# Kernel tuning notes

Hardware: AMD Instinct MI355X
Metric: run time of the kernel (lower is better)

The kernel has to match this reference:

```python
import jax, jax.numpy as jnp
import numpy as np

EPS = 1e-5

def setup_inputs() -> dict:
    key = jax.random.key(0)
    ks = jax.random.split(key, 12)
    b, C, Hx = 8, 1024, 28          # x: (b, C, Hx, Hx); y: (b, C//2, 2*Hx, 2*Hx)
    C2 = C // 2
    r = C2 // 7                      # fc bottleneck = 73
    f32 = jnp.float32
    inp = {
        'y': jax.random.normal(ks[0], (b, C2, 2*Hx, 2*Hx), f32),
        'x': jax.random.normal(ks[1], (b, C, Hx, Hx), f32),
        'fc1_w': jax.random.normal(ks[2], (r, C2), f32) * 0.02,
        'fc2_w': jax.random.normal(ks[3], (C2, r), f32) * 0.02,
        'conv_w': jax.random.normal(ks[4], (C2, C, 1, 1), f32) * 0.02,
        'conv_b': jnp.zeros((C2,), f32),
        'conv1_w': jax.random.normal(ks[5], (C2, C2 * 4, 1, 1), f32) * 0.02,
        'conv1_b': jnp.zeros((C2,), f32),
        'bn_gamma': jnp.ones((C2,), f32),
        'bn_beta': jnp.zeros((C2,), f32),
        'bn_mean': jnp.zeros((C2,), f32),
        'bn_var': jnp.ones((C2,), f32),
        'dw_w': jax.random.normal(ks[6], (C, 1, 3, 3), f32) * 0.1,  # depthwise, groups=C
        'dw_b': jnp.zeros((C,), f32),
    }
    return inp

def reference(y, x, fc1_w, fc2_w, conv_w, conv_b, conv1_w, conv1_b,
              bn_gamma, bn_beta, bn_mean, bn_var, dw_w, dw_b):
    def bn(t):  # BatchNorm2d in eval mode (running stats); same bn module reused twice
        return (t - bn_mean[:, None, None]) * jax.lax.rsqrt(bn_var[:, None, None] + EPS) \
               * bn_gamma[:, None, None] + bn_beta[:, None, None]
    # SE channel attention on y
    s = jnp.mean(y, axis=(2, 3))                              # (b, C2) GAP
    s = jax.nn.relu(s @ fc1_w.T) @ fc2_w.T                    # bias-free FCs
    y1 = y * jax.nn.sigmoid(s)[:, :, None, None]
    # depthwise 3x3 conv on x
    x1 = jax.lax.conv_general_dilated(
        x, dw_w, (1, 1), ((1, 1), (1, 1)),
        feature_group_count=x.shape[1],
        dimension_numbers=('NCHW', 'OIHW', 'NCHW')) + dw_b[None, :, None, None]
    # np.cov per (b, c) map: rows are variables, ddof=1 -> (Xc @ Xc^T)/(W-1)
    Wn = x1.shape[-1]
    xc = x1 - jnp.mean(x1, axis=-1, keepdims=True)
    x2 = jnp.einsum('bchw,bcgw->bchg', xc, xc) / (Wn - 1)     # (b, C, H, H)
    # 1x1 conv C->C2, bn, sigmoid
    x2 = jnp.einsum('bchw,oc->bohw', x2, conv_w[:, :, 0, 0]) + conv_b[None, :, None, None]
    x2 = jax.nn.sigmoid(bn(x2))
    # bilinear upsample x2 (half-pixel == torch align_corners=False)
    def up2(t):
        bb, cc, hh, ww = t.shape
        return jax.image.resize(t, (bb, cc, 2 * hh, 2 * ww), method='bilinear')
    x_up = up2(x)
    x2_up = up2(x2)
    cat = jnp.concatenate([y1, x2_up, x_up], axis=1)          # (b, 4*C2, 2H, 2W)
    out = jnp.einsum('bchw,oc->bohw', cat, conv1_w[:, :, 0, 0]) + conv1_b[None, :, None, None]
    return jax.nn.relu(bn(out))
```

## Files before the change

### kernel.cpp

```cpp
#include <hip/hip_runtime.h>
#include <math.h>

#define EPSV 1e-5f
#define B 8
#define C 1024
#define C2 512
#define RK 73
#define HW 784
#define QW 3136

typedef __attribute__((ext_vector_type(8))) short bf16x8;
typedef __attribute__((ext_vector_type(4))) float f32x4;

__device__ __forceinline__ unsigned short f2bf(float f) {
    unsigned u = __float_as_uint(f);
    return (unsigned short)((u + 0x7fffu + ((u >> 16) & 1u)) >> 16);
}
__device__ __forceinline__ float ld_f(const float* p) { return *p; }
__device__ __forceinline__ float ld_f(const unsigned short* p) {
    return __uint_as_float(((unsigned)*p) << 16);
}

__global__ void gap_kernel(const float* __restrict__ y, float* __restrict__ s0) {
    int bc = blockIdx.x;
    const float* p = y + (size_t)bc * QW;
    float sum = 0.f;
    for (int i = threadIdx.x; i < QW; i += 256) sum += p[i];
    for (int off = 32; off > 0; off >>= 1) sum += __shfl_down(sum, off, 64);
    __shared__ float red[4];
    if ((threadIdx.x & 63) == 0) red[threadIdx.x >> 6] = sum;
    __syncthreads();
    if (threadIdx.x == 0)
        s0[bc] = (red[0] + red[1] + red[2] + red[3]) * (1.0f / QW);
}

__global__ void se_fc_kernel(const float* __restrict__ s0,
                             const float* __restrict__ fc1_w,
                             const float* __restrict__ fc2_w,
                             float* __restrict__ att) {
    int b = blockIdx.x;
    __shared__ float sv[C2];
    __shared__ float hv[RK];
    for (int i = threadIdx.x; i < C2; i += 256) sv[i] = s0[b * C2 + i];
    __syncthreads();
    if (threadIdx.x < RK) {
        float acc = 0.f;
        const float* wr = fc1_w + threadIdx.x * C2;
        for (int k = 0; k < C2; ++k) acc += wr[k] * sv[k];
        hv[threadIdx.x] = fmaxf(acc, 0.f);
    }
    __syncthreads();
    for (int o = threadIdx.x; o < C2; o += 256) {
        float acc = 0.f;
        const float* wr = fc2_w + o * RK;
        for (int j = 0; j < RK; ++j) acc += wr[j] * hv[j];
        att[b * C2 + o] = 1.f / (1.f + expf(-acc));
    }
}

__global__ void dwcov_kernel(const float* __restrict__ x,
                             const float* __restrict__ dw_w,
                             const float* __restrict__ dw_b,
                             unsigned short* __restrict__ cov) {
    int bc = blockIdx.x;
    int c = bc & (C - 1);
    __shared__ float xs[HW];
    __shared__ float x1[HW];
    __shared__ float rm[28];
    const float* px = x + (size_t)bc * HW;
    for (int i = threadIdx.x; i < HW; i += 256) xs[i] = px[i];
    float wk[9];
#pragma unroll
    for (int j = 0; j < 9; ++j) wk[j] = dw_w[c * 9 + j];
    float bias = dw_b[c];
    __syncthreads();
    for (int p = threadIdx.x; p < HW; p += 256) {
        int h = p / 28, w = p - h * 28;
        float acc = bias;
#pragma unroll
        for (int dh = 0; dh < 3; ++dh) {
            int hh = h + dh - 1;
            if (hh < 0 || hh >= 28) continue;
#pragma unroll
            for (int dw = 0; dw < 3; ++dw) {
                int ww = w + dw - 1;
                if (ww < 0 || ww >= 28) continue;
                acc += xs[hh * 28 + ww] * wk[dh * 3 + dw];
            }
        }
        x1[p] = acc;
    }
    __syncthreads();
    if (threadIdx.x < 28) {
        float s = 0.f;
        for (int w = 0; w < 28; ++w) s += x1[threadIdx.x * 28 + w];
        rm[threadIdx.x] = s * (1.f / 28.f);
    }
    __syncthreads();
    unsigned short* pc = cov + (size_t)bc * HW;
    for (int p = threadIdx.x; p < HW; p += 256) {
        int h = p / 28, g = p - h * 28;
        float mh = rm[h], mg = rm[g];
        float acc = 0.f;
        for (int w = 0; w < 28; ++w)
            acc += (x1[h * 28 + w] - mh) * (x1[g * 28 + w] - mg);
        pc[p] = f2bf(acc * (1.f / 27.f));
    }
}

__global__ void pack_w(const float* __restrict__ conv_w, const float* __restrict__ conv_b,
                       const float* __restrict__ conv1_w, const float* __restrict__ conv1_b,
                       const float* __restrict__ bn_g, const float* __restrict__ bn_b,
                       const float* __restrict__ bn_m, const float* __restrict__ bn_v,
                       const float* __restrict__ att,
                       unsigned short* __restrict__ w0b, unsigned short* __restrict__ w1y,
                       unsigned short* __restrict__ w1pT,
                       float* __restrict__ sA, float* __restrict__ sB0, float* __restrict__ sB1) {
    int o = blockIdx.x, t = threadIdx.x;
    for (int i = t; i < C; i += 256) w0b[(size_t)o * C + i] = f2bf(conv_w[(size_t)o * C + i]);
    for (int i = t; i < 1536; i += 256) w1pT[(size_t)o * 1536 + i] = f2bf(conv1_w[(size_t)o * 2048 + 512 + i]);
#pragma unroll
    for (int b = 0; b < B; ++b)
        for (int c = t; c < C2; c += 256)
            w1y[((size_t)b * C2 + o) * C2 + c] = f2bf(conv1_w[(size_t)o * 2048 + c] * att[b * C2 + c]);
    if (t == 0) {
        float sc = rsqrtf(bn_v[o] + EPSV) * bn_g[o];
        float bi = bn_b[o] - bn_m[o] * sc;
        sA[o] = sc;
        sB0[o] = conv_b[o] * sc + bi;
        sB1[o] = conv1_b[o] * sc + bi;
    }
}

__global__ __launch_bounds__(256)
void transpose_pass(const float* __restrict__ src, unsigned short* __restrict__ dst,
                    int rows, int cols, int dpitch, int doff) {
    int b = blockIdx.z;
    int c0 = blockIdx.y * 64, p0 = blockIdx.x * 64;
    __shared__ float ts[64][65];
    int tid = threadIdx.x;
    int pl = tid & 63, r0 = tid >> 6;
    const float* sb = src + ((size_t)b * rows + c0) * cols + p0;
    if (p0 + pl < cols) {
#pragma unroll
        for (int j = 0; j < 16; ++j) {
            int cl = r0 + j * 4;
            ts[cl][pl] = sb[(size_t)cl * cols + pl];
        }
    }
    __syncthreads();
    int cl = tid & 63;
#pragma unroll
    for (int j = 0; j < 16; ++j) {
        int pl2 = r0 + j * 4;
        if (p0 + pl2 < cols)
            dst[((size_t)b * cols + p0 + pl2) * dpitch + doff + c0 + cl] = f2bf(ts[cl][pl2]);
    }
}

template<int MODE, int K>
__global__ __launch_bounds__(256)
void mfma_gemm(const unsigned short* __restrict__ wpk,
               const void* __restrict__ bsrc_v,
               const unsigned short* __restrict__ Pb,
               const float* __restrict__ sA, const float* __restrict__ sB,
               void* __restrict__ outv) {
    constexpr int NIT = K / 32;
    constexpr int NT  = (MODE == 2) ? 49 : 98;
    constexpr int TPC = (NT + 7) / 8;
    int bx = blockIdx.x;
    int r = bx & 7, i = bx >> 3;
    int t = r * TPC + (i >> 3);
    if (t >= NT) return;
    int o0 = (i & 7) * 64;
    int n0 = t * 64;
    int b = blockIdx.z;
    union SM {
        struct { __align__(16) unsigned short Wt[2][2560]; __align__(16) unsigned short At[2][2560]; } s;
        float pt[(MODE == 2) ? 64 * 84 : 4];
    };
    __shared__ SM sm;
    int tid = threadIdx.x;
    int lane = tid & 63, wv = tid >> 6;
    int ln = lane & 15, quad = lane >> 4;
    int o_w = (wv >> 1) * 32, q_w = (wv & 1) * 32;
    int swr = tid >> 2, swk = (tid & 3) * 8;
    int s_gq = tid & 63, s_gk8 = tid >> 6;
    int qg = n0 + s_gq;
    const unsigned short* wp = (MODE == 2) ? wpk + (size_t)b * C2 * C2 : wpk;
    const unsigned short* wg = wp + (size_t)(o0 + swr) * K + swk;
    const unsigned short* bg_s = nullptr;
    const unsigned short* bg_c = nullptr;
    const float* bg_f = nullptr;
    if (MODE == 0) {
        int bq = qg / HW, pp = qg - bq * HW;
        bg_s = (const unsigned short*)bsrc_v + ((size_t)bq * C + s_gk8 * 8) * HW + pp;
    } else if (MODE == 1) {
        bg_c = (const unsigned short*)bsrc_v + (size_t)(n0 + swr) * K + swk;
    } else {
        bg_f = (const float*)bsrc_v + ((size_t)b * C2 + s_gk8 * 8) * QW + qg;
    }

    {
        float4 wv4 = *(const float4*)wg;
        *(float4*)&sm.s.Wt[0][swr * 40 + swk] = wv4;
        unsigned short pk[8];
        if (MODE == 0) {
#pragma unroll
            for (int j = 0; j < 8; ++j) pk[j] = bg_s[(size_t)j * HW];
            *(float4*)&sm.s.At[0][s_gq * 40 + s_gk8 * 8] = *(float4*)pk;
        } else if (MODE == 1) {
            *(float4*)&sm.s.At[0][swr * 40 + swk] = *(const float4*)bg_c;
        } else {
#pragma unroll
            for (int j = 0; j < 8; ++j) pk[j] = f2bf(bg_f[(size_t)j * QW]);
            *(float4*)&sm.s.At[0][s_gq * 40 + s_gk8 * 8] = *(float4*)pk;
        }
    }
    __syncthreads();

    f32x4 acc[2][2] = {};
    for (int i2 = 0; i2 < NIT; ++i2) {
        int cur = i2 & 1;
        float4 wn;
        unsigned short bn[8];
        if (i2 + 1 < NIT) {
            wn = *(const float4*)(wg + (size_t)(i2 + 1) * 32);
            if (MODE == 0) {
                const unsigned short* s = bg_s + (size_t)(i2 + 1) * 32 * HW;
#pragma unroll
                for (int j = 0; j < 8; ++j) bn[j] = s[(size_t)j * HW];
            } else if (MODE == 1) {
                *(float4*)bn = *(const float4*)(bg_c + (size_t)(i2 + 1) * 32);
            } else {
                const float* s = bg_f + (size_t)(i2 + 1) * 32 * QW;
#pragma unroll
                for (int j = 0; j < 8; ++j) bn[j] = f2bf(s[(size_t)j * QW]);
            }
        }
        bf16x8 af[2], bfr[2];
#pragma unroll
        for (int mt = 0; mt < 2; ++mt)
            af[mt] = *(const bf16x8*)&sm.s.Wt[cur][(o_w + mt * 16 + ln) * 40 + quad * 8];
#pragma unroll
        for (int nt = 0; nt < 2; ++nt)
            bfr[nt] = *(const bf16x8*)&sm.s.At[cur][(q_w + nt * 16 + ln) * 40 + quad * 8];
#pragma unroll
        for (int mt = 0; mt < 2; ++mt)
#pragma unroll
            for (int nt = 0; nt < 2; ++nt)
                acc[mt][nt] = __builtin_amdgcn_mfma_f32_16x16x32_bf16(af[mt], bfr[nt], acc[mt][nt], 0, 0, 0);
        if (i2 + 1 < NIT) {
            int nxt = cur ^ 1;
            *(float4*)&sm.s.Wt[nxt][swr * 40 + swk] = wn;
            if (MODE == 1) *(float4*)&sm.s.At[nxt][swr * 40 + swk] = *(float4*)bn;
            else           *(float4*)&sm.s.At[nxt][s_gq * 40 + s_gk8 * 8] = *(float4*)bn;
            __syncthreads();
        }
    }

    if (MODE == 2) {
        float* outp = (float*)outv;
        __syncthreads();
        int h0 = n0 / 56;
        int hmin = (h0 & 1) ? (h0 >> 1) : max(0, (h0 >> 1) - 1);
        for (int e = tid; e < 64 * 84; e += 256) {
            int o_l = e / 84, rem = e - o_l * 84;
            int s = rem / 28, w = rem - s * 28;
            int row = min(hmin + s, 27);
            sm.pt[e] = ld_f(&Pb[((size_t)b * C2 + o0 + o_l) * HW + row * 28 + w]);
        }
        __syncthreads();
#pragma unroll
        for (int nt = 0; nt < 2; ++nt) {
            int q = n0 + q_w + nt * 16 + ln;
            int hq = q / 56, wq = q - hq * 56;
            int hm = hq >> 1, wm = wq >> 1;
            int hn = (hq & 1) ? min(hm + 1, 27) : max(hm - 1, 0);
            int wn_ = (wq & 1) ? min(wm + 1, 27) : max(wm - 1, 0);
            int rm_ = (hm - hmin) * 28, rn_ = (hn - hmin) * 28;
#pragma unroll
            for (int mt = 0; mt < 2; ++mt)
#pragma unroll
                for (int reg = 0; reg < 4; ++reg) {
                    int ol = o_w + mt * 16 + quad * 4 + reg;
                    int o = o0 + ol;
                    const float* Pt = &sm.pt[ol * 84];
                    float up = 0.5625f * Pt[rm_ + wm] + 0.1875f * (Pt[rm_ + wn_] + Pt[rn_ + wm])
                             + 0.0625f * Pt[rn_ + wn_];
                    float v = (acc[mt][nt][reg] + up) * sA[o] + sB[o];
                    outp[((size_t)b * C2 + o) * QW + q] = fmaxf(v, 0.f);
                }
        }
    } else if (MODE == 0) {
        unsigned short* outp = (unsigned short*)outv;
#pragma unroll
        for (int nt = 0; nt < 2; ++nt) {
            int n = n0 + q_w + nt * 16 + ln;
#pragma unroll
            for (int mt = 0; mt < 2; ++mt) {
                int ob = o0 + o_w + mt * 16 + quad * 4;
                unsigned short pk[4];
#pragma unroll
                for (int reg = 0; reg < 4; ++reg) {
                    int o = ob + reg;
                    float v = acc[mt][nt][reg] * sA[o] + sB[o];
                    pk[reg] = f2bf(1.f / (1.f + expf(-v)));
                }
                *(uint2*)&outp[(size_t)n * 1536 + ob] = *(uint2*)pk;
            }
        }
    } else {
        unsigned short* outp = (unsigned short*)outv;
#pragma unroll
        for (int nt = 0; nt < 2; ++nt) {
            int n = n0 + q_w + nt * 16 + ln;
            int be = n / HW, pe = n - be * HW;
#pragma unroll
            for (int mt = 0; mt < 2; ++mt)
#pragma unroll
                for (int reg = 0; reg < 4; ++reg) {
                    int o = o0 + o_w + mt * 16 + quad * 4 + reg;
                    outp[((size_t)be * C2 + o) * HW + pe] = f2bf(acc[mt][nt][reg]);
                }
        }
    }
}

extern "C" void kernel_launch(void* const* d_in, const int* in_sizes, int n_in,
                              void* d_out, int out_size, void* d_ws, size_t ws_size,
                              hipStream_t stream) {
    const float* y       = (const float*)d_in[0];
    const float* x       = (const float*)d_in[1];
    const float* fc1_w   = (const float*)d_in[2];
    const float* fc2_w   = (const float*)d_in[3];
    const float* conv_w  = (const float*)d_in[4];
    const float* conv_b  = (const float*)d_in[5];
    const float* conv1_w = (const float*)d_in[6];
    const float* conv1_b = (const float*)d_in[7];
    const float* bn_g    = (const float*)d_in[8];
    const float* bn_b    = (const float*)d_in[9];
    const float* bn_m    = (const float*)d_in[10];
    const float* bn_v    = (const float*)d_in[11];
    const float* dw_w    = (const float*)d_in[12];
    const float* dw_b    = (const float*)d_in[13];
    float* out = (float*)d_out;

    float* ws  = (float*)d_ws;
    float* s0  = ws;
    float* att = ws + 4096;
    float* sA  = ws + 8192;
    float* sB0 = ws + 8704;
    float* sB1 = ws + 9216;
    unsigned short* w0b    = (unsigned short*)(ws + 9728);
    unsigned short* w1y    = w0b + (size_t)C2 * C;
    unsigned short* w1pT   = w1y + (size_t)B * C2 * C2;
    unsigned short* cov_bf = w1pT + (size_t)C2 * 1536;
    unsigned short* BcatT  = cov_bf + (size_t)B * C * HW;
    unsigned short* Pb     = BcatT + (size_t)B * HW * 1536;

    gap_kernel<<<B * C2, 256, 0, stream>>>(y, s0);
    se_fc_kernel<<<B, 256, 0, stream>>>(s0, fc1_w, fc2_w, att);
    pack_w<<<C2, 256, 0, stream>>>(conv_w, conv_b, conv1_w, conv1_b,
                                   bn_g, bn_b, bn_m, bn_v, att,
                                   w0b, w1y, w1pT, sA, sB0, sB1);
    dwcov_kernel<<<B * C, 256, 0, stream>>>(x, dw_w, dw_b, cov_bf);
    transpose_pass<<<dim3(13, 16, B), 256, 0, stream>>>(x, BcatT, C, HW, 1536, 512);
    mfma_gemm<0, 1024><<<dim3(832), 256, 0, stream>>>(w0b, cov_bf, nullptr, sA, sB0, BcatT);
    mfma_gemm<1, 1536><<<dim3(832), 256, 0, stream>>>(w1pT, BcatT, nullptr, sA, sB0, Pb);
    mfma_gemm<2, 512><<<dim3(448, 1, B), 256, 0, stream>>>(w1y, y, Pb, sA, sB1, out);
}
```

Measured before the change: 333.4 us.

## Double GEMM output-channel tile to 128 and use packed bf16 conversion

Each GEMM block now covers 128 output channels instead of 64, with every wave computing a 64x32 sub-tile (4x2 MFMA tiles), and the grid is halved to match. Each B-operand tile loaded from global memory is therefore reused across twice as many output channels, cutting redundant loads of the strided activation data, most notably the fp32 y input in the final GEMM. The fp32-to-bf16 conversion for y now uses the packed v_cvt_pk_bf16_f32 instruction instead of manual rounding. In exchange, registers and LDS per block go up and the block count drops, which lowers occupancy and parallelism.

```diff
diff --git a/kernel.cpp b/kernel.cpp
--- a/kernel.cpp
+++ b/kernel.cpp
@@ -15,6 +15,11 @@
 __device__ __forceinline__ unsigned short f2bf(float f) {
     unsigned u = __float_as_uint(f);
     return (unsigned short)((u + 0x7fffu + ((u >> 16) & 1u)) >> 16);
+}
+__device__ __forceinline__ unsigned cvt_pk_bf16(float lo, float hi) {
+    unsigned r;
+    asm("v_cvt_pk_bf16_f32 %0, %1, %2" : "=v"(r) : "v"(lo), "v"(hi));
+    return r;
 }
 __device__ __forceinline__ float ld_f(const float* p) { return *p; }
 __device__ __forceinline__ float ld_f(const unsigned short* p) {
@@ -169,26 +174,27 @@
     constexpr int NT  = (MODE == 2) ? 49 : 98;
     constexpr int TPC = (NT + 7) / 8;
     int bx = blockIdx.x;
-    int r = bx & 7, i = bx >> 3;
-    int t = r * TPC + (i >> 3);
+    int r = bx & 7, ii = bx >> 3;
+    int t = r * TPC + (ii >> 2);
     if (t >= NT) return;
-    int o0 = (i & 7) * 64;
+    int o0 = (ii & 3) * 128;
     int n0 = t * 64;
     int b = blockIdx.z;
     union SM {
-        struct { __align__(16) unsigned short Wt[2][2560]; __align__(16) unsigned short At[2][2560]; } s;
-        float pt[(MODE == 2) ? 64 * 84 : 4];
+        struct { __align__(16) unsigned short Wt[2][5120]; __align__(16) unsigned short At[2][2560]; } s;
+        float pt[(MODE == 2) ? 128 * 84 : 4];
     };
     __shared__ SM sm;
     int tid = threadIdx.x;
     int lane = tid & 63, wv = tid >> 6;
     int ln = lane & 15, quad = lane >> 4;
-    int o_w = (wv >> 1) * 32, q_w = (wv & 1) * 32;
+    int o_w = (wv >> 1) * 64, q_w = (wv & 1) * 32;
     int swr = tid >> 2, swk = (tid & 3) * 8;
     int s_gq = tid & 63, s_gk8 = tid >> 6;
     int qg = n0 + s_gq;
     const unsigned short* wp = (MODE == 2) ? wpk + (size_t)b * C2 * C2 : wpk;
     const unsigned short* wg = wp + (size_t)(o0 + swr) * K + swk;
+    const unsigned short* wg2 = wg + (size_t)64 * K;
     const unsigned short* bg_s = nullptr;
     const unsigned short* bg_c = nullptr;
     const float* bg_f = nullptr;
@@ -203,29 +209,35 @@
 
     {
         float4 wv4 = *(const float4*)wg;
+        float4 wv5 = *(const float4*)wg2;
         *(float4*)&sm.s.Wt[0][swr * 40 + swk] = wv4;
-        unsigned short pk[8];
+        *(float4*)&sm.s.Wt[0][(64 + swr) * 40 + swk] = wv5;
         if (MODE == 0) {
+            unsigned short pk[8];
 #pragma unroll
             for (int j = 0; j < 8; ++j) pk[j] = bg_s[(size_t)j * HW];
             *(float4*)&sm.s.At[0][s_gq * 40 + s_gk8 * 8] = *(float4*)pk;
         } else if (MODE == 1) {
             *(float4*)&sm.s.At[0][swr * 40 + swk] = *(const float4*)bg_c;
         } else {
-#pragma unroll
-            for (int j = 0; j < 8; ++j) pk[j] = f2bf(bg_f[(size_t)j * QW]);
-            *(float4*)&sm.s.At[0][s_gq * 40 + s_gk8 * 8] = *(float4*)pk;
-        }
-    }
-    __syncthreads();
-
-    f32x4 acc[2][2] = {};
+            unsigned pk2[4];
+#pragma unroll
+            for (int j = 0; j < 4; ++j)
+                pk2[j] = cvt_pk_bf16(bg_f[(size_t)(2 * j) * QW], bg_f[(size_t)(2 * j + 1) * QW]);
+            *(float4*)&sm.s.At[0][s_gq * 40 + s_gk8 * 8] = *(float4*)pk2;
+        }
+    }
+    __syncthreads();
+
+    f32x4 acc[4][2] = {};
     for (int i2 = 0; i2 < NIT; ++i2) {
         int cur = i2 & 1;
-        float4 wn;
+        float4 wnA, wnB;
         unsigned short bn[8];
+        unsigned bn2[4];
         if (i2 + 1 < NIT) {
-            wn = *(const float4*)(wg + (size_t)(i2 + 1) * 32);
+            wnA = *(const float4*)(wg + (size_t)(i2 + 1) * 32);
+            wnB = *(const float4*)(wg2 + (size_t)(i2 + 1) * 32);
             if (MODE == 0) {
                 const unsigned short* s = bg_s + (size_t)(i2 + 1) * 32 * HW;
 #pragma unroll
@@ -235,26 +247,29 @@
             } else {
                 const float* s = bg_f + (size_t)(i2 + 1) * 32 * QW;
 #pragma unroll
-                for (int j = 0; j < 8; ++j) bn[j] = f2bf(s[(size_t)j * QW]);
+                for (int j = 0; j < 4; ++j)
+                    bn2[j] = cvt_pk_bf16(s[(size_t)(2 * j) * QW], s[(size_t)(2 * j + 1) * QW]);
             }
         }
-        bf16x8 af[2], bfr[2];
-#pragma unroll
-        for (int mt = 0; mt < 2; ++mt)
+        bf16x8 af[4], bfr[2];
+#pragma unroll
+        for (int mt = 0; mt < 4; ++mt)
             af[mt] = *(const bf16x8*)&sm.s.Wt[cur][(o_w + mt * 16 + ln) * 40 + quad * 8];
 #pragma unroll
         for (int nt = 0; nt < 2; ++nt)
             bfr[nt] = *(const bf16x8*)&sm.s.At[cur][(q_w + nt * 16 + ln) * 40 + quad * 8];
 #pragma unroll
-        for (int mt = 0; mt < 2; ++mt)
+        for (int mt = 0; mt < 4; ++mt)
 #pragma unroll
             for (int nt = 0; nt < 2; ++nt)
                 acc[mt][nt] = __builtin_amdgcn_mfma_f32_16x16x32_bf16(af[mt], bfr[nt], acc[mt][nt], 0, 0, 0);
         if (i2 + 1 < NIT) {
             int nxt = cur ^ 1;
-            *(float4*)&sm.s.Wt[nxt][swr * 40 + swk] = wn;
-            if (MODE == 1) *(float4*)&sm.s.At[nxt][swr * 40 + swk] = *(float4*)bn;
-            else           *(float4*)&sm.s.At[nxt][s_gq * 40 + s_gk8 * 8] = *(float4*)bn;
+            *(float4*)&sm.s.Wt[nxt][swr * 40 + swk] = wnA;
+            *(float4*)&sm.s.Wt[nxt][(64 + swr) * 40 + swk] = wnB;
+            if (MODE == 1)      *(float4*)&sm.s.At[nxt][swr * 40 + swk] = *(float4*)bn;
+            else if (MODE == 0) *(float4*)&sm.s.At[nxt][s_gq * 40 + s_gk8 * 8] = *(float4*)bn;
+            else                *(float4*)&sm.s.At[nxt][s_gq * 40 + s_gk8 * 8] = *(float4*)bn2;
             __syncthreads();
         }
     }
@@ -264,7 +279,7 @@
         __syncthreads();
         int h0 = n0 / 56;
         int hmin = (h0 & 1) ? (h0 >> 1) : max(0, (h0 >> 1) - 1);
-        for (int e = tid; e < 64 * 84; e += 256) {
+        for (int e = tid; e < 128 * 84; e += 256) {
             int o_l = e / 84, rem = e - o_l * 84;
             int s = rem / 28, w = rem - s * 28;
             int row = min(hmin + s, 27);
@@ -280,7 +295,7 @@
             int wn_ = (wq & 1) ? min(wm + 1, 27) : max(wm - 1, 0);
             int rm_ = (hm - hmin) * 28, rn_ = (hn - hmin) * 28;
 #pragma unroll
-            for (int mt = 0; mt < 2; ++mt)
+            for (int mt = 0; mt < 4; ++mt)
 #pragma unroll
                 for (int reg = 0; reg < 4; ++reg) {
                     int ol = o_w + mt * 16 + quad * 4 + reg;
@@ -298,7 +313,7 @@
         for (int nt = 0; nt < 2; ++nt) {
             int n = n0 + q_w + nt * 16 + ln;
 #pragma unroll
-            for (int mt = 0; mt < 2; ++mt) {
+            for (int mt = 0; mt < 4; ++mt) {
                 int ob = o0 + o_w + mt * 16 + quad * 4;
                 unsigned short pk[4];
 #pragma unroll
@@ -317,7 +332,7 @@
             int n = n0 + q_w + nt * 16 + ln;
             int be = n / HW, pe = n - be * HW;
 #pragma unroll
-            for (int mt = 0; mt < 2; ++mt)
+            for (int mt = 0; mt < 4; ++mt)
 #pragma unroll
                 for (int reg = 0; reg < 4; ++reg) {
                     int o = o0 + o_w + mt * 16 + quad * 4 + reg;
@@ -366,7 +381,7 @@
                                    w0b, w1y, w1pT, sA, sB0, sB1);
     dwcov_kernel<<<B * C, 256, 0, stream>>>(x, dw_w, dw_b, cov_bf);
     transpose_pass<<<dim3(13, 16, B), 256, 0, stream>>>(x, BcatT, C, HW, 1536, 512);
-    mfma_gemm<0, 1024><<<dim3(832), 256, 0, stream>>>(w0b, cov_bf, nullptr, sA, sB0, BcatT);
-    mfma_gemm<1, 1536><<<dim3(832), 256, 0, stream>>>(w1pT, BcatT, nullptr, sA, sB0, Pb);
-    mfma_gemm<2, 512><<<dim3(448, 1, B), 256, 0, stream>>>(w1y, y, Pb, sA, sB1, out);
-}
+    mfma_gemm<0, 1024><<<dim3(416), 256, 0, stream>>>(w0b, cov_bf, nullptr, sA, sB0, BcatT);
+    mfma_gemm<1, 1536><<<dim3(416), 256, 0, stream>>>(w1pT, BcatT, nullptr, sA, sB0, Pb);
+    mfma_gemm<2, 512><<<dim3(224, 1, B), 256, 0, stream>>>(w1y, y, Pb, sA, sB1, out);
+}
```

Result: no change. 332.6 us (-0.2%).

## Deepen MFMA GEMM prefetch to two stages in registers with manual barriers

Applied to the files above, without the earlier changes.

Restructures the bf16 MFMA GEMM main loop so global loads are issued two K-chunks ahead into two register stage sets, and the float-to-bf16 conversion is deferred until the LDS store. The loop is unrolled by two with explicit lgkmcnt waits, raw s_barrier and sched_barrier in place of __syncthreads. It uses the packed v_cvt_pk_bf16_f32 instruction instead of a manual rounding routine, and it spreads leftover N-tiles evenly across the 8 block groups instead of padding the last group. The goal is to hide global load latency and cut conversion ALU work, at the cost of more registers and a loop that assumes NIT is even.

```diff
diff --git a/kernel.cpp b/kernel.cpp
--- a/kernel.cpp
+++ b/kernel.cpp
@@ -15,6 +15,11 @@
 __device__ __forceinline__ unsigned short f2bf(float f) {
     unsigned u = __float_as_uint(f);
     return (unsigned short)((u + 0x7fffu + ((u >> 16) & 1u)) >> 16);
+}
+__device__ __forceinline__ unsigned cvt_pk_bf16(float lo, float hi) {
+    unsigned r;
+    asm("v_cvt_pk_bf16_f32 %0, %1, %2" : "=v"(r) : "v"(lo), "v"(hi));
+    return r;
 }
 __device__ __forceinline__ float ld_f(const float* p) { return *p; }
 __device__ __forceinline__ float ld_f(const unsigned short* p) {
@@ -167,12 +172,14 @@
                void* __restrict__ outv) {
     constexpr int NIT = K / 32;
     constexpr int NT  = (MODE == 2) ? 49 : 98;
-    constexpr int TPC = (NT + 7) / 8;
+    constexpr int QN = NT >> 3, REM = NT & 7;
     int bx = blockIdx.x;
-    int r = bx & 7, i = bx >> 3;
-    int t = r * TPC + (i >> 3);
-    if (t >= NT) return;
-    int o0 = (i & 7) * 64;
+    int r = bx & 7, ii = bx >> 3;
+    int og = ii & 7, s = ii >> 3;
+    int cnt = QN + (r < REM ? 1 : 0);
+    if (s >= cnt) return;
+    int t = (r < REM ? r * (QN + 1) : REM * (QN + 1) + (r - REM) * QN) + s;
+    int o0 = og * 64;
     int n0 = t * 64;
     int b = blockIdx.z;
     union SM {
@@ -201,63 +208,78 @@
         bg_f = (const float*)bsrc_v + ((size_t)b * C2 + s_gk8 * 8) * QW + qg;
     }
 
-    {
-        float4 wv4 = *(const float4*)wg;
-        *(float4*)&sm.s.Wt[0][swr * 40 + swk] = wv4;
-        unsigned short pk[8];
-        if (MODE == 0) {
-#pragma unroll
-            for (int j = 0; j < 8; ++j) pk[j] = bg_s[(size_t)j * HW];
-            *(float4*)&sm.s.At[0][s_gq * 40 + s_gk8 * 8] = *(float4*)pk;
-        } else if (MODE == 1) {
-            *(float4*)&sm.s.At[0][swr * 40 + swk] = *(const float4*)bg_c;
-        } else {
-#pragma unroll
-            for (int j = 0; j < 8; ++j) pk[j] = f2bf(bg_f[(size_t)j * QW]);
-            *(float4*)&sm.s.At[0][s_gq * 40 + s_gk8 * 8] = *(float4*)pk;
-        }
-    }
-    __syncthreads();
+    uint4 stA_a, stB_a;
+    uint4 stA_b, stB_b;
+    unsigned stA_h[8], stB_h[8];
+    float stA_f[8], stB_f[8];
+
+#define LD_STAGE(P, CH) {                                                   \
+        P##_a = *(const uint4*)(wg + (size_t)(CH) * 32);                    \
+        if (MODE == 0) {                                                    \
+            const unsigned short* _p = bg_s + (size_t)(CH) * 32 * HW;       \
+            _Pragma("unroll")                                               \
+            for (int _j = 0; _j < 8; ++_j) P##_h[_j] = _p[(size_t)_j * HW]; \
+        } else if (MODE == 1) {                                             \
+            P##_b = *(const uint4*)(bg_c + (size_t)(CH) * 32);              \
+        } else {                                                            \
+            const float* _p = bg_f + (size_t)(CH) * 32 * QW;                \
+            _Pragma("unroll")                                               \
+            for (int _j = 0; _j < 8; ++_j) P##_f[_j] = _p[(size_t)_j * QW]; \
+        } }
+
+#define ST_STAGE(P, BUF) {                                                  \
+        *(uint4*)&sm.s.Wt[BUF][swr * 40 + swk] = P##_a;                     \
+        if (MODE == 1) {                                                    \
+            *(uint4*)&sm.s.At[BUF][swr * 40 + swk] = P##_b;                 \
+        } else if (MODE == 0) {                                             \
+            uint4 _v;                                                       \
+            _v.x = P##_h[0] | (P##_h[1] << 16);                             \
+            _v.y = P##_h[2] | (P##_h[3] << 16);                             \
+            _v.z = P##_h[4] | (P##_h[5] << 16);                             \
+            _v.w = P##_h[6] | (P##_h[7] << 16);                             \
+            *(uint4*)&sm.s.At[BUF][s_gq * 40 + s_gk8 * 8] = _v;             \
+        } else {                                                            \
+            uint4 _v;                                                       \
+            _v.x = cvt_pk_bf16(P##_f[0], P##_f[1]);                         \
+            _v.y = cvt_pk_bf16(P##_f[2], P##_f[3]);                         \
+            _v.z = cvt_pk_bf16(P##_f[4], P##_f[5]);                         \
+            _v.w = cvt_pk_bf16(P##_f[6], P##_f[7]);                         \
+            *(uint4*)&sm.s.At[BUF][s_gq * 40 + s_gk8 * 8] = _v;             \
+        } }
+
+#define GEMM_BODY(BUF, P, CHW, CHL) {                                               \
+        bf16x8 af0 = *(const bf16x8*)&sm.s.Wt[BUF][(o_w + ln) * 40 + quad * 8];     \
+        bf16x8 af1 = *(const bf16x8*)&sm.s.Wt[BUF][(o_w + 16 + ln) * 40 + quad * 8];\
+        bf16x8 bf0 = *(const bf16x8*)&sm.s.At[BUF][(q_w + ln) * 40 + quad * 8];     \
+        bf16x8 bf1 = *(const bf16x8*)&sm.s.At[BUF][(q_w + 16 + ln) * 40 + quad * 8];\
+        acc[0][0] = __builtin_amdgcn_mfma_f32_16x16x32_bf16(af0, bf0, acc[0][0], 0, 0, 0); \
+        acc[0][1] = __builtin_amdgcn_mfma_f32_16x16x32_bf16(af0, bf1, acc[0][1], 0, 0, 0); \
+        acc[1][0] = __builtin_amdgcn_mfma_f32_16x16x32_bf16(af1, bf0, acc[1][0], 0, 0, 0); \
+        acc[1][1] = __builtin_amdgcn_mfma_f32_16x16x32_bf16(af1, bf1, acc[1][1], 0, 0, 0); \
+        if ((CHW) < NIT) {                                                          \
+            ST_STAGE(P, (BUF) ^ 1)                                                  \
+            if ((CHL) < NIT) LD_STAGE(P, (CHL))                                     \
+            asm volatile("s_waitcnt lgkmcnt(0)" ::: "memory");                      \
+            __builtin_amdgcn_s_barrier();                                           \
+            __builtin_amdgcn_sched_barrier(0);                                      \
+        } }
+
+    LD_STAGE(stA, 0)
+    ST_STAGE(stA, 0)
+    LD_STAGE(stA, 1)
+    if (2 < NIT) LD_STAGE(stB, 2)
+    asm volatile("s_waitcnt lgkmcnt(0)" ::: "memory");
+    __builtin_amdgcn_s_barrier();
+    __builtin_amdgcn_sched_barrier(0);
 
     f32x4 acc[2][2] = {};
-    for (int i2 = 0; i2 < NIT; ++i2) {
-        int cur = i2 & 1;
-        float4 wn;
-        unsigned short bn[8];
-        if (i2 + 1 < NIT) {
-            wn = *(const float4*)(wg + (size_t)(i2 + 1) * 32);
-            if (MODE == 0) {
-                const unsigned short* s = bg_s + (size_t)(i2 + 1) * 32 * HW;
-#pragma unroll
-                for (int j = 0; j < 8; ++j) bn[j] = s[(size_t)j * HW];
-            } else if (MODE == 1) {
-                *(float4*)bn = *(const float4*)(bg_c + (size_t)(i2 + 1) * 32);
-            } else {
-                const float* s = bg_f + (size_t)(i2 + 1) * 32 * QW;
-#pragma unroll
-                for (int j = 0; j < 8; ++j) bn[j] = f2bf(s[(size_t)j * QW]);
-            }
-        }
-        bf16x8 af[2], bfr[2];
-#pragma unroll
-        for (int mt = 0; mt < 2; ++mt)
-            af[mt] = *(const bf16x8*)&sm.s.Wt[cur][(o_w + mt * 16 + ln) * 40 + quad * 8];
-#pragma unroll
-        for (int nt = 0; nt < 2; ++nt)
-            bfr[nt] = *(const bf16x8*)&sm.s.At[cur][(q_w + nt * 16 + ln) * 40 + quad * 8];
-#pragma unroll
-        for (int mt = 0; mt < 2; ++mt)
-#pragma unroll
-            for (int nt = 0; nt < 2; ++nt)
-                acc[mt][nt] = __builtin_amdgcn_mfma_f32_16x16x32_bf16(af[mt], bfr[nt], acc[mt][nt], 0, 0, 0);
-        if (i2 + 1 < NIT) {
-            int nxt = cur ^ 1;
-            *(float4*)&sm.s.Wt[nxt][swr * 40 + swk] = wn;
-            if (MODE == 1) *(float4*)&sm.s.At[nxt][swr * 40 + swk] = *(float4*)bn;
-            else           *(float4*)&sm.s.At[nxt][s_gq * 40 + s_gk8 * 8] = *(float4*)bn;
-            __syncthreads();
-        }
-    }
+    for (int i2 = 0; i2 < NIT; i2 += 2) {
+        GEMM_BODY(0, stA, i2 + 1, i2 + 3)
+        GEMM_BODY(1, stB, i2 + 2, i2 + 4)
+    }
+#undef GEMM_BODY
+#undef ST_STAGE
+#undef LD_STAGE
 
     if (MODE == 2) {
         float* outp = (float*)outv;
@@ -266,8 +288,8 @@
         int hmin = (h0 & 1) ? (h0 >> 1) : max(0, (h0 >> 1) - 1);
         for (int e = tid; e < 64 * 84; e += 256) {
             int o_l = e / 84, rem = e - o_l * 84;
-            int s = rem / 28, w = rem - s * 28;
-            int row = min(hmin + s, 27);
+            int s2 = rem / 28, w = rem - s2 * 28;
+            int row = min(hmin + s2, 27);
             sm.pt[e] = ld_f(&Pb[((size_t)b * C2 + o0 + o_l) * HW + row * 28 + w]);
         }
         __syncthreads();
```

After: 320.3 us. 1.04x faster.
